# Kernel optimization log

Hardware: AMD Instinct MI355X
Metric: run time of the kernel (lower is better)

The kernel has to match this reference:

```python
import jax, jax.numpy as jnp
import numpy as np
from jax.scipy.special import gammaln

D = 512       # feature_dim
C = 64        # n classes (n-way)
SHOTS = 5     # matches hardcoded self.fix_Nj = 5
Q = 2048      # query samples
FIX_NJ = 5.0


def setup_inputs() -> dict:
    key = jax.random.key(0)
    k1, k2 = jax.random.split(key, 2)
    X_support = jax.random.normal(k1, (C * SHOTS, D), dtype=jnp.float32)
    # labels 0..C-1, SHOTS contiguous samples per class (required: code indexes mu[j] by label)
    y = (jnp.arange(C * SHOTS, dtype=jnp.int32) // SHOTS)
    X_query = jax.random.normal(k2, (Q, D), dtype=jnp.float32)
    # learned parameters, initialized exactly as in the torch module
    m = jnp.zeros((1, D), dtype=jnp.float32)
    kappa = jnp.float32(0.1)
    nu = jnp.float32(D)
    triu_S_diag = jnp.ones((D,), dtype=jnp.float32)
    triu_S_lower = jnp.eye(D, dtype=jnp.float32)
    return {"X_support": X_support, "y": y, "X_query": X_query,
            "m": m, "kappa": kappa, "nu": nu,
            "triu_S_diag": triu_S_diag, "triu_S_lower": triu_S_lower}


def reference(X_support, y, X_query, m, kappa, nu, triu_S_diag, triu_S_lower):
    # ---- compute_shared_part ----
    # triu(ones,1).t() == strictly-lower-triangular mask
    mask = jnp.tril(jnp.ones((D, D), dtype=X_support.dtype), -1)
    L = jnp.diag(jnp.abs(triu_S_diag)) + triu_S_lower * mask
    kappa_n = jnp.abs(kappa) + 1e-6 + FIX_NJ
    m_with_weight = jnp.abs(kappa + 1e-6) / kappa_n * m          # [1,D]
    xmean_weight = FIX_NJ / kappa_n
    scatter = L @ L.T                                            # self_outer(L), square case
    sp = jnp.clip(nu, D - 1 + 1e-6) + FIX_NJ - D + 2             # sharedpart (scalar)
    bias_shared = gammaln(0.5 * (sp + D)) - gammaln(0.5 * sp) - 0.5 * D * jnp.log(sp)

    # ---- fit_image_label, batched over classes ----
    # y is arange//SHOTS so grouping X[y==j] == contiguous reshape
    Xc = X_support.reshape(C, SHOTS, D)                          # [C,S,D]
    x_mean = Xc.mean(axis=1)                                     # [C,D]
    mean_outer = jnp.einsum('csd,cse->cde', Xc, Xc) / SHOTS      # X_j^T X_j / N_j
    mu = m_with_weight + x_mean * xmean_weight                   # [C,D]
    dm = x_mean - m                                              # [C,D]; self_outer of [1,D] row -> outer product
    sigma = scatter[None] + mean_outer \
        + jnp.einsum('cd,ce->cde', dm, dm) * ((jnp.abs(kappa) + 1e-6) / kappa_n)
    sigma = sigma / ((kappa_n + 1) / (kappa_n * sp))             # [C,D,D]
    sigma_inv = jnp.linalg.inv(sigma)                            # batched inverse
    _, logdet = jnp.linalg.slogdet(sigma)                        # sigma is PD -> logdet
    biases = bias_shared - 0.5 * logdet                          # [C]

    # ---- predict, batched over queries and classes ----
    diff = X_query[:, None, :] - mu[None, :, :]                  # [Q,C,D]
    tmp = jnp.einsum('qcd,cde->qce', diff, sigma_inv)
    dist = jnp.sum(tmp * diff, axis=-1)                          # Mahalanobis [Q,C]
    return biases[None, :] - 0.5 * (sp + D) * jnp.log(1.0 + dist / sp)
```

## Files before the change

kernel.cpp:

```cpp
#include <hip/hip_runtime.h>
#include <math.h>

#define D 512
#define NC 64
#define NQ 2048

typedef unsigned short u16;
typedef __attribute__((ext_vector_type(8))) short bf8;
typedef __attribute__((ext_vector_type(4))) float f4;

#define OFF_S    0
#define OFF_ABH  32
#define OFF_ABL  (OFF_ABH + 655360)
#define OFF_LH   (OFF_ABL + 655360)
#define OFF_LL   (OFF_LH + 131072)
#define OFF_WH   (OFF_LL + 131072)
#define OFF_WL   (OFF_WH + 131072)
#define OFF_YYH  (OFF_WL + 131072)
#define OFF_YYL  (OFF_YYH + 655360)
#define OFF_AQ   (OFF_YYL + 655360)
#define OFF_GRAM (OFF_AQ + NQ)

#define GIX(i, j) ((i) * 7 - (i) * ((i) + 1) / 2 + (j))

__device__ inline float wred(float v) {
#pragma unroll
  for (int off = 32; off; off >>= 1) v += __shfl_down(v, off);
  return v;
}

__device__ inline void split2(float v, u16& h, u16& l) {
  unsigned u = __float_as_uint(v);
  h = (u16)(u >> 16);
  float hf = __uint_as_float(u & 0xFFFF0000u);
  float r = v - hf;
  unsigned ru = __float_as_uint(r);
  l = (u16)((ru + 0x7FFFu + ((ru >> 16) & 1u)) >> 16);
}

__device__ inline void split4(float a0, float a1, float a2, float a3,
                              ushort4& h, ushort4& l) {
  u16 hh, ll;
  split2(a0, hh, ll); h.x = hh; l.x = ll;
  split2(a1, hh, ll); h.y = hh; l.y = ll;
  split2(a2, hh, ll); h.z = hh; l.z = ll;
  split2(a3, hh, ll); h.w = hh; l.w = ll;
}

#define MPAD 68
template <int N>
__device__ inline void lds_mm(float (*M)[MPAD], int ar, int ac, int br, int bc,
                              int cr, int cc, bool neg) {
  const int T = N / 16;
  int tx = (threadIdx.x & 15) * T, ty = (threadIdx.x >> 4) * T;
  float acc[T][T];
#pragma unroll
  for (int i = 0; i < T; ++i)
#pragma unroll
    for (int j = 0; j < T; ++j) acc[i][j] = 0.f;
#pragma unroll 8
  for (int k = 0; k < N; ++k) {
    float a[T], b[T];
#pragma unroll
    for (int i = 0; i < T; ++i) a[i] = M[ar + ty + i][ac + k];
#pragma unroll
    for (int j = 0; j < T; ++j) b[j] = M[br + k][bc + tx + j];
#pragma unroll
    for (int i = 0; i < T; ++i)
#pragma unroll
      for (int j = 0; j < T; ++j) acc[i][j] += a[i] * b[j];
  }
#pragma unroll
  for (int i = 0; i < T; ++i)
#pragma unroll
    for (int j = 0; j < T; ++j)
      M[cr + ty + i][cc + tx + j] = neg ? -acc[i][j] : acc[i][j];
}

__device__ inline void inv64(float (*M)[MPAD], int tid) {
  {
    float x[16];
    int q = tid >> 4, col = tid & 15;
    if (tid < 64) {
      int b = q << 4;
#pragma unroll
      for (int i = 0; i < 16; ++i) {
        float acc = 0.f;
#pragma unroll
        for (int k = 0; k < i; ++k) acc += M[b + i][b + k] * x[k];
        x[i] = (((i == col) ? 1.f : 0.f) - acc) / M[b + i][b + i];
      }
    }
    __syncthreads();
    if (tid < 64) {
      int b = q << 4;
#pragma unroll
      for (int i = 0; i < 16; ++i) M[b + i][b + col] = x[i];
    }
    __syncthreads();
  }
  for (int pp = 0; pp < 2; ++pp) {
    int r0 = 32 * pp;
    lds_mm<16>(M, r0 + 16, r0, r0, r0, r0, r0 + 16, false);
  }
  __syncthreads();
  for (int pp = 0; pp < 2; ++pp) {
    int r0 = 32 * pp;
    lds_mm<16>(M, r0 + 16, r0 + 16, r0, r0 + 16, r0 + 16, r0, true);
  }
  __syncthreads();
  for (int idx = tid; idx < 512; idx += 256) {
    int t2 = idx >> 8, r = (idx >> 4) & 15, c = idx & 15;
    M[32 * t2 + r][32 * t2 + 16 + c] = 0.f;
  }
  __syncthreads();
  lds_mm<32>(M, 32, 0, 0, 0, 0, 32, false);
  __syncthreads();
  lds_mm<32>(M, 32, 32, 0, 32, 32, 0, true);
  __syncthreads();
  for (int idx = tid; idx < 1024; idx += 256) {
    int r = idx >> 5, c = idx & 31;
    M[r][32 + c] = 0.f;
  }
  __syncthreads();
}

__global__ __launch_bounds__(256) void k_prep(const float* __restrict__ diag,
                                              const float* __restrict__ low,
                                              const float* __restrict__ Xs,
                                              const float* __restrict__ Xq,
                                              const float* __restrict__ m,
                                              const float* __restrict__ kp,
                                              const float* __restrict__ nup,
                                              u16* __restrict__ Lh, u16* __restrict__ Ll,
                                              u16* __restrict__ ABh, u16* __restrict__ ABl,
                                              u16* __restrict__ Wh, u16* __restrict__ Wl,
                                              float* __restrict__ S, float* __restrict__ aq,
                                              float* __restrict__ Gram) {
  __shared__ float M[64][MPAD];
  int bid = blockIdx.x, tid = threadIdx.x;
  if (bid < 8) {
    int p = bid * 64;
    for (int idx = tid; idx < 4096; idx += 256) {
      int r = idx >> 6, c = idx & 63;
      float v;
      if (r == c)      v = fabsf(diag[p + r]);
      else if (r > c)  v = low[(size_t)(p + r) * D + p + c];
      else             v = 0.f;
      M[r][c] = v;
    }
    __syncthreads();
    inv64(M, tid);
    for (int idx = tid; idx < 1024; idx += 256) {
      int r = idx >> 4, c4 = (idx & 15) << 2;
      ushort4 hh, ll;
      split4(M[r][c4 + 0], M[r][c4 + 1], M[r][c4 + 2], M[r][c4 + 3], hh, ll);
      size_t gi = (size_t)(p + r) * D + p + c4;
      *reinterpret_cast<ushort4*>(Wh + gi) = hh;
      *reinterpret_cast<ushort4*>(Wl + gi) = ll;
    }
  } else if (bid < 72) {
    int c = bid - 8;
    if (tid < 128) {
      float kappa = kp[0];
      float kn = fabsf(kappa) + 1e-6f + 5.0f;
      float xw = 5.0f / kn;
      float mw = fabsf(kappa + 1e-6f) / kn;
      float sw = sqrtf((fabsf(kappa) + 1e-6f) / kn);
      const float is5 = 0.44721359549995793f;
      int d4 = tid;
      float xs[5][4];
#pragma unroll
      for (int s = 0; s < 5; ++s) {
        float4 v = reinterpret_cast<const float4*>(Xs + (size_t)(c * 5 + s) * D)[d4];
        xs[s][0] = v.x; xs[s][1] = v.y; xs[s][2] = v.z; xs[s][3] = v.w;
      }
      float4 mvv = reinterpret_cast<const float4*>(m)[d4];
      float mv[4] = {mvv.x, mvv.y, mvv.z, mvv.w};
      float rows[8][4];
#pragma unroll
      for (int e = 0; e < 4; ++e) {
        float xm = (xs[0][e] + xs[1][e] + xs[2][e] + xs[3][e] + xs[4][e]) * 0.2f;
#pragma unroll
        for (int s = 0; s < 5; ++s) rows[s][e] = xs[s][e] * is5;
        rows[5][e] = sw * (xm - mv[e]);
        rows[6][e] = mw * mv[e] + xw * xm;
        rows[7][e] = 0.f;
      }
#pragma unroll
      for (int s = 0; s < 8; ++s) {
        ushort4 hh, ll;
        split4(rows[s][0], rows[s][1], rows[s][2], rows[s][3], hh, ll);
        size_t gi = (size_t)(c * 8 + s) * D + 4 * tid;
        *reinterpret_cast<ushort4*>(ABh + gi) = hh;
        *reinterpret_cast<ushort4*>(ABl + gi) = ll;
      }
    }
  } else if (bid == 72) {
    for (int i = tid; i < NQ; i += 256) aq[i] = 0.f;
    for (int i = tid; i < NC * 28; i += 256) Gram[i] = 0.f;
    if (tid >= 64) return;
    float part = 0.f;
    for (int i = tid; i < D; i += 64) part += logf(fabsf(diag[i]));
    part = wred(part);
    if (tid != 0) return;
    float lda = 2.f * part;
    float kappa = kp[0], nu = nup[0];
    float kn = fabsf(kappa) + 1e-6f + 5.0f;
    float sp = fmaxf(nu, (float)(D - 1) + 1e-6f) + 5.0f - (float)D + 2.0f;
    float bias_shared = lgammaf(0.5f * (sp + (float)D)) - lgammaf(0.5f * sp)
                      - 0.5f * (float)D * logf(sp);
    float scale = kn * sp / (kn + 1.0f);
    S[3] = bias_shared;
    S[8] = 1.f / scale;
    S[9] = (float)D * logf(scale) + lda;
    S[10] = 0.5f * (sp + (float)D);
    S[11] = 1.f / sp;
  } else if (bid < 329) {
    int t = (bid - 73) * 1024 + tid * 4;
    int i = t >> 9, j = t & 511;
    float4 lv = *reinterpret_cast<const float4*>(low + t);
    float a[4] = {lv.x, lv.y, lv.z, lv.w};
    float dv = diag[i];
    float o[4];
#pragma unroll
    for (int e = 0; e < 4; ++e) {
      int jj = j + e;
      o[e] = (i == jj) ? fabsf(dv) : (i > jj ? a[e] : 0.f);
    }
    ushort4 hh, ll;
    split4(o[0], o[1], o[2], o[3], hh, ll);
    *reinterpret_cast<ushort4*>(Lh + t) = hh;
    *reinterpret_cast<ushort4*>(Ll + t) = ll;
  } else {
    size_t base = (size_t)(bid - 329) * 8192;
#pragma unroll
    for (int it = 0; it < 8; ++it) {
      size_t idx = base + it * 1024 + tid * 4;
      float4 v = *reinterpret_cast<const float4*>(Xq + idx);
      ushort4 hh, ll;
      split4(v.x, v.y, v.z, v.w, hh, ll);
      *reinterpret_cast<ushort4*>(ABh + (size_t)512 * D + idx) = hh;
      *reinterpret_cast<ushort4*>(ABl + (size_t)512 * D + idx) = ll;
    }
  }
}

__global__ __launch_bounds__(256) void k_solve(const u16* __restrict__ Lh,
                                               const u16* __restrict__ Ll,
                                               u16* __restrict__ Wh,
                                               const u16* __restrict__ Wl) {
  __shared__ __align__(16) u16 XTh[32][520];
  __shared__ __align__(16) u16 XTl[32][520];
  __shared__ __align__(16) u16 STh[32][72];
  __shared__ __align__(16) u16 STl[32][72];
  int J = blockIdx.x;
  int i0 = J >> 1;
  int tid = threadIdx.x, w = tid >> 6, lane = tid & 63;
  int lr = lane & 15, kq = lane >> 4;
  for (int idx = tid; idx < 64 * 32; idx += 256) {
    int r = idx >> 5, c = idx & 31;
    size_t gi = (size_t)(64 * i0 + r) * D + 64 * i0 + (J & 1) * 32 + c;
    XTh[c][64 * i0 + r] = Wh[gi];
    XTl[c][64 * i0 + r] = Wl[gi];
  }
  __syncthreads();
  for (int i = i0 + 1; i < 8; ++i) {
    f4 acc[2];
    acc[0] = (f4){0.f, 0.f, 0.f, 0.f};
    acc[1] = (f4){0.f, 0.f, 0.f, 0.f};
    for (int k = i0; k < i; ++k) {
#pragma unroll
      for (int kk = 0; kk < 2; ++kk) {
        size_t ga = (size_t)(64 * i + w * 16 + lr) * D + 64 * k + kk * 32 + kq * 8;
        bf8 ah = *reinterpret_cast<const bf8*>(Lh + ga);
        bf8 al = *reinterpret_cast<const bf8*>(Ll + ga);
#pragma unroll
        for (int nf = 0; nf < 2; ++nf) {
          bf8 bh = *reinterpret_cast<const bf8*>(&XTh[nf * 16 + lr][64 * k + kk * 32 + kq * 8]);
          bf8 bl = *reinterpret_cast<const bf8*>(&XTl[nf * 16 + lr][64 * k + kk * 32 + kq * 8]);
          acc[nf] = __builtin_amdgcn_mfma_f32_16x16x32_bf16(ah, bh, acc[nf], 0, 0, 0);
          acc[nf] = __builtin_amdgcn_mfma_f32_16x16x32_bf16(ah, bl, acc[nf], 0, 0, 0);
          acc[nf] = __builtin_amdgcn_mfma_f32_16x16x32_bf16(al, bh, acc[nf], 0, 0, 0);
        }
      }
    }
#pragma unroll
    for (int nf = 0; nf < 2; ++nf)
#pragma unroll
      for (int reg = 0; reg < 4; ++reg) {
        float v = -acc[nf][reg];
        u16 hh, ll; split2(v, hh, ll);
        int c = nf * 16 + lr, r = w * 16 + kq * 4 + reg;
        STh[c][r] = hh; STl[c][r] = ll;
      }
    __syncthreads();
    f4 acc2[2];
    acc2[0] = (f4){0.f, 0.f, 0.f, 0.f};
    acc2[1] = (f4){0.f, 0.f, 0.f, 0.f};
#pragma unroll
    for (int kk = 0; kk < 2; ++kk) {
      size_t ga = (size_t)(64 * i + w * 16 + lr) * D + 64 * i + kk * 32 + kq * 8;
      bf8 ah = *reinterpret_cast<const bf8*>(Wh + ga);
      bf8 al = *reinterpret_cast<const bf8*>(Wl + ga);
#pragma unroll
      for (int nf = 0; nf < 2; ++nf) {
        bf8 bh = *reinterpret_cast<const bf8*>(&STh[nf * 16 + lr][kk * 32 + kq * 8]);
        bf8 bl = *reinterpret_cast<const bf8*>(&STl[nf * 16 + lr][kk * 32 + kq * 8]);
        acc2[nf] = __builtin_amdgcn_mfma_f32_16x16x32_bf16(ah, bh, acc2[nf], 0, 0, 0);
        acc2[nf] = __builtin_amdgcn_mfma_f32_16x16x32_bf16(ah, bl, acc2[nf], 0, 0, 0);
        acc2[nf] = __builtin_amdgcn_mfma_f32_16x16x32_bf16(al, bh, acc2[nf], 0, 0, 0);
      }
    }
#pragma unroll
    for (int nf = 0; nf < 2; ++nf)
#pragma unroll
      for (int reg = 0; reg < 4; ++reg) {
        float v = acc2[nf][reg];
        u16 hh, ll; split2(v, hh, ll);
        int r = w * 16 + kq * 4 + reg, c = nf * 16 + lr;
        Wh[(size_t)(64 * i + r) * D + 32 * J + c] = hh;
        XTh[c][64 * i + r] = hh; XTl[c][64 * i + r] = ll;
      }
    __syncthreads();
  }
}

__global__ __launch_bounds__(256) void k_mf1(const u16* __restrict__ ABh, const u16* __restrict__ ABl,
                                             const u16* __restrict__ Wh,
                                             u16* __restrict__ YYh, u16* __restrict__ YYl,
                                             float* __restrict__ Gram, float* __restrict__ aq) {
  __shared__ float Csh[64][68];
  int tid = threadIdx.x, w = tid >> 6, lane = tid & 63;
  int bn = (7 - (int)blockIdx.x) * 64;
  int m0 = blockIdx.y * 64 + w * 16;
  int lr = lane & 15, kof = (lane >> 4) * 8;
  const u16* ah_p = ABh + (size_t)(m0 + lr) * D + kof;
  const u16* al_p = ABl + (size_t)(m0 + lr) * D + kof;
  const u16* bh_p = Wh + (size_t)(bn + lr) * D + kof;
  f4 acc[4];
#pragma unroll
  for (int nf = 0; nf < 4; ++nf) acc[nf] = (f4){0.f, 0.f, 0.f, 0.f};
  int Klim = bn + 64;
#pragma unroll 2
  for (int k0 = 0; k0 < Klim; k0 += 32) {
    bf8 ah = *reinterpret_cast<const bf8*>(ah_p + k0);
    bf8 al = *reinterpret_cast<const bf8*>(al_p + k0);
    bf8 bh[4];
#pragma unroll
    for (int nf = 0; nf < 4; ++nf)
      bh[nf] = *reinterpret_cast<const bf8*>(bh_p + (size_t)nf * 16 * D + k0);
#pragma unroll
    for (int nf = 0; nf < 4; ++nf)
      acc[nf] = __builtin_amdgcn_mfma_f32_16x16x32_bf16(ah, bh[nf], acc[nf], 0, 0, 0);
#pragma unroll
    for (int nf = 0; nf < 4; ++nf)
      acc[nf] = __builtin_amdgcn_mfma_f32_16x16x32_bf16(al, bh[nf], acc[nf], 0, 0, 0);
  }
  int rbase = m0 + ((lane >> 4) << 2);
#pragma unroll
  for (int reg = 0; reg < 4; ++reg) {
    int row = rbase + reg;
    float sq = 0.f;
#pragma unroll
    for (int nf = 0; nf < 4; ++nf) {
      float v = acc[nf][reg];
      size_t gi = (size_t)row * D + bn + nf * 16 + lr;
      u16 hh, ll; split2(v, hh, ll);
      YYh[gi] = hh;
      if (row >= 512) YYl[gi] = ll;
      sq += v * v;
    }
    if (row >= 512) {
#pragma unroll
      for (int mk = 1; mk < 16; mk <<= 1) sq += __shfl_xor(sq, mk);
      if (lr == 0) atomicAdd(&aq[row - 512], sq);
    }
  }
  if (blockIdx.y < 8) {
#pragma unroll
    for (int reg = 0; reg < 4; ++reg)
#pragma unroll
      for (int nf = 0; nf < 4; ++nf)
        Csh[w * 16 + ((lane >> 4) << 2) + reg][nf * 16 + lr] = acc[nf][reg];
    __syncthreads();
    if (tid < 224) {
      const int PI[28] = {0,0,0,0,0,0,0, 1,1,1,1,1,1, 2,2,2,2,2, 3,3,3,3, 4,4,4, 5,5, 6};
      const int PJ[28] = {0,1,2,3,4,5,6, 1,2,3,4,5,6, 2,3,4,5,6, 3,4,5,6, 4,5,6, 5,6, 6};
      int cl = tid / 28, p = tid % 28;
      const float* ri = Csh[cl * 8 + PI[p]];
      const float* rj = Csh[cl * 8 + PJ[p]];
      float s = 0.f;
#pragma unroll
      for (int c4 = 0; c4 < 64; c4 += 4) {
        float4 a = *reinterpret_cast<const float4*>(&ri[c4]);
        float4 b = *reinterpret_cast<const float4*>(&rj[c4]);
        s += a.x * b.x + a.y * b.y + a.z * b.z + a.w * b.w;
      }
      atomicAdd(&Gram[(blockIdx.y * 8 + cl) * 28 + p], s);
    }
  }
}

__global__ __launch_bounds__(256) void k_mf2(const u16* __restrict__ Yh, const u16* __restrict__ Yl,
                                             const u16* __restrict__ Bh,
                                             const float* __restrict__ aq,
                                             const float* __restrict__ Gram,
                                             const float* __restrict__ S,
                                             float* __restrict__ out) {
  __shared__ float Csh[4][16][68];
  __shared__ float PRo[8][15], PRd[8][6], Psv[8][6], Pb[8], Ph[8];
  int tid = threadIdx.x, w = tid >> 6, lane = tid & 63;
  int m0 = blockIdx.x * 64 + w * 16;
  int bn = blockIdx.y * 64;
  int lr = lane & 15, kof = (lane >> 4) * 8;
  const u16* ah_p = Yh + (size_t)(m0 + lr) * D + kof;
  const u16* al_p = Yl + (size_t)(m0 + lr) * D + kof;
  const u16* bh_p = Bh + (size_t)(bn + lr) * D + kof;
  f4 acc[4];
#pragma unroll
  for (int nf = 0; nf < 4; ++nf) acc[nf] = (f4){0.f, 0.f, 0.f, 0.f};
#pragma unroll 2
  for (int k0 = 0; k0 < D; k0 += 32) {
    bf8 ah = *reinterpret_cast<const bf8*>(ah_p + k0);
    bf8 al = *reinterpret_cast<const bf8*>(al_p + k0);
    bf8 bh[4];
#pragma unroll
    for (int nf = 0; nf < 4; ++nf)
      bh[nf] = *reinterpret_cast<const bf8*>(bh_p + (size_t)nf * 16 * D + k0);
#pragma unroll
    for (int nf = 0; nf < 4; ++nf)
      acc[nf] = __builtin_amdgcn_mfma_f32_16x16x32_bf16(ah, bh[nf], acc[nf], 0, 0, 0);
#pragma unroll
    for (int nf = 0; nf < 4; ++nf)
      acc[nf] = __builtin_amdgcn_mfma_f32_16x16x32_bf16(al, bh[nf], acc[nf], 0, 0, 0);
  }
#pragma unroll
  for (int reg = 0; reg < 4; ++reg)
#pragma unroll
    for (int nf = 0; nf < 4; ++nf)
      Csh[w][((lane >> 4) << 2) + reg][nf * 16 + lr] = acc[nf][reg];
  if (tid < 8) {
    int c = blockIdx.y * 8 + tid;
    float Gv[28];
#pragma unroll
    for (int p = 0; p < 28; ++p) Gv[p] = Gram[c * 28 + p];
    float R[6][6];
    float logdetM = 0.f;
#pragma unroll
    for (int i = 0; i < 6; ++i) {
      float s = Gv[GIX(i, i)] + 1.f;
#pragma unroll
      for (int k = 0; k < i; ++k) s -= R[i][k] * R[i][k];
      float rii = sqrtf(s);
      R[i][i] = rii;
      logdetM += logf(rii);
      float inv = 1.f / rii;
      PRd[tid][i] = inv;
#pragma unroll
      for (int r = i + 1; r < 6; ++r) {
        float s2 = Gv[GIX(i, r)];
#pragma unroll
        for (int k = 0; k < i; ++k) s2 -= R[r][k] * R[i][k];
        R[r][i] = s2 * inv;
      }
    }
#pragma unroll
    for (int i = 1; i < 6; ++i)
#pragma unroll
      for (int k = 0; k < i; ++k)
        PRo[tid][i * (i - 1) / 2 + k] = R[i][k];
#pragma unroll
    for (int j = 0; j < 6; ++j) Psv[tid][j] = Gv[GIX(j, 6)];
    Ph[tid] = Gv[27];
    Pb[tid] = S[3] - 0.5f * (S[9] + 2.f * logdetM);
  }
  __syncthreads();
  float s8 = S[8], s10 = S[10], s11 = S[11];
  int r = lr;
  int q = m0 + r;
  float aqv = aq[q];
#pragma unroll
  for (int cc = 0; cc < 2; ++cc) {
    int cl = ((lane >> 4) << 1) + cc;
    const float* t = &Csh[w][r][cl * 8];
    float e[6];
#pragma unroll
    for (int j = 0; j < 6; ++j) e[j] = t[j] - Psv[cl][j];
    const float* o = PRo[cl];
    const float* dg = PRd[cl];
    float z0 = e[0] * dg[0];
    float z1 = (e[1] - o[0] * z0) * dg[1];
    float z2 = (e[2] - o[1] * z0 - o[2] * z1) * dg[2];
    float z3 = (e[3] - o[3] * z0 - o[4] * z1 - o[5] * z2) * dg[3];
    float z4 = (e[4] - o[6] * z0 - o[7] * z1 - o[8] * z2 - o[9] * z3) * dg[4];
    float z5 = (e[5] - o[10] * z0 - o[11] * z1 - o[12] * z2 - o[13] * z3 - o[14] * z4) * dg[5];
    float quad = z0 * z0 + z1 * z1 + z2 * z2 + z3 * z3 + z4 * z4 + z5 * z5;
    float dist = (aqv - 2.f * t[6] + Ph[cl] - quad) * s8;
    out[(size_t)q * NC + blockIdx.y * 8 + cl] = Pb[cl] - s10 * log1pf(dist * s11);
  }
}

extern "C" void kernel_launch(void* const* d_in, const int* in_sizes, int n_in,
                              void* d_out, int out_size, void* d_ws, size_t ws_size,
                              hipStream_t stream) {
  const float* Xs   = (const float*)d_in[0];
  const float* Xq   = (const float*)d_in[2];
  const float* m    = (const float*)d_in[3];
  const float* kap  = (const float*)d_in[4];
  const float* nu   = (const float*)d_in[5];
  const float* diag = (const float*)d_in[6];
  const float* low  = (const float*)d_in[7];
  float* ws = (float*)d_ws;

  float* S    = ws + OFF_S;
  u16*   ABh  = (u16*)(ws + OFF_ABH);
  u16*   ABl  = (u16*)(ws + OFF_ABL);
  u16*   Lh   = (u16*)(ws + OFF_LH);
  u16*   Ll   = (u16*)(ws + OFF_LL);
  u16*   Wh   = (u16*)(ws + OFF_WH);
  u16*   Wl   = (u16*)(ws + OFF_WL);
  u16*   YYh  = (u16*)(ws + OFF_YYH);
  u16*   YYl  = (u16*)(ws + OFF_YYL);
  float* aq   = ws + OFF_AQ;
  float* Gram = ws + OFF_GRAM;

  hipLaunchKernelGGL(k_prep, dim3(457), dim3(256), 0, stream,
                     diag, low, Xs, Xq, m, kap, nu, Lh, Ll, ABh, ABl, Wh, Wl, S, aq, Gram);
  hipLaunchKernelGGL(k_solve, dim3(16), dim3(256), 0, stream, Lh, Ll, Wh, Wl);
  hipLaunchKernelGGL(k_mf1, dim3(8, 40), dim3(256), 0, stream,
                     ABh, ABl, Wh, YYh, YYl, Gram, aq);
  hipLaunchKernelGGL(k_mf2, dim3(32, 8), dim3(256), 0, stream,
                     YYh + (size_t)512 * D, YYl + (size_t)512 * D, YYh,
                     aq, Gram, S, (float*)d_out);
}
```

Before: 88.79 us.

## Replace explicit L inverse and GEMM with fused blockwise triangular solve

Instead of forming the full inverse of L (k_solve) and then multiplying the support and query rows by it (k_mf1), each block now loads 32 rows into LDS and does a blocked forward substitution using L and the inverted 64x64 diagonal blocks. The Gram partial sums and query squared norms are computed in the same kernel, and the prep kernel no longer writes the bf16 split copies of the inputs. This drops one launch and several global round trips. In exchange only 80 blocks run a serial 8-step dependency chain with many barriers, so the GPU may be underfilled.

```diff
diff --git a/kernel.cpp b/kernel.cpp
--- a/kernel.cpp
+++ b/kernel.cpp
@@ -10,13 +10,11 @@
 typedef __attribute__((ext_vector_type(4))) float f4;
 
 #define OFF_S    0
-#define OFF_ABH  32
-#define OFF_ABL  (OFF_ABH + 655360)
-#define OFF_LH   (OFF_ABL + 655360)
+#define OFF_LH   32
 #define OFF_LL   (OFF_LH + 131072)
-#define OFF_WH   (OFF_LL + 131072)
-#define OFF_WL   (OFF_WH + 131072)
-#define OFF_YYH  (OFF_WL + 131072)
+#define OFF_DIH  (OFF_LL + 131072)
+#define OFF_DIL  (OFF_DIH + 16384)
+#define OFF_YYH  (OFF_DIL + 16384)
 #define OFF_YYL  (OFF_YYH + 655360)
 #define OFF_AQ   (OFF_YYL + 655360)
 #define OFF_GRAM (OFF_AQ + NQ)
@@ -47,6 +45,10 @@
   split2(a3, hh, ll); h.w = hh; l.w = ll;
 }
 
+__device__ inline float recon(u16 h, u16 l) {
+  return __uint_as_float((unsigned)h << 16) + __uint_as_float((unsigned)l << 16);
+}
+
 #define MPAD 68
 template <int N>
 __device__ inline void lds_mm(float (*M)[MPAD], int ar, int ac, int br, int bc,
@@ -127,16 +129,11 @@
 
 __global__ __launch_bounds__(256) void k_prep(const float* __restrict__ diag,
                                               const float* __restrict__ low,
-                                              const float* __restrict__ Xs,
-                                              const float* __restrict__ Xq,
-                                              const float* __restrict__ m,
                                               const float* __restrict__ kp,
                                               const float* __restrict__ nup,
                                               u16* __restrict__ Lh, u16* __restrict__ Ll,
-                                              u16* __restrict__ ABh, u16* __restrict__ ABl,
-                                              u16* __restrict__ Wh, u16* __restrict__ Wl,
-                                              float* __restrict__ S, float* __restrict__ aq,
-                                              float* __restrict__ Gram) {
+                                              u16* __restrict__ DIh, u16* __restrict__ DIl,
+                                              float* __restrict__ S) {
   __shared__ float M[64][MPAD];
   int bid = blockIdx.x, tid = threadIdx.x;
   if (bid < 8) {
@@ -155,50 +152,27 @@
       int r = idx >> 4, c4 = (idx & 15) << 2;
       ushort4 hh, ll;
       split4(M[r][c4 + 0], M[r][c4 + 1], M[r][c4 + 2], M[r][c4 + 3], hh, ll);
-      size_t gi = (size_t)(p + r) * D + p + c4;
-      *reinterpret_cast<ushort4*>(Wh + gi) = hh;
-      *reinterpret_cast<ushort4*>(Wl + gi) = ll;
-    }
-  } else if (bid < 72) {
-    int c = bid - 8;
-    if (tid < 128) {
-      float kappa = kp[0];
-      float kn = fabsf(kappa) + 1e-6f + 5.0f;
-      float xw = 5.0f / kn;
-      float mw = fabsf(kappa + 1e-6f) / kn;
-      float sw = sqrtf((fabsf(kappa) + 1e-6f) / kn);
-      const float is5 = 0.44721359549995793f;
-      int d4 = tid;
-      float xs[5][4];
-#pragma unroll
-      for (int s = 0; s < 5; ++s) {
-        float4 v = reinterpret_cast<const float4*>(Xs + (size_t)(c * 5 + s) * D)[d4];
-        xs[s][0] = v.x; xs[s][1] = v.y; xs[s][2] = v.z; xs[s][3] = v.w;
-      }
-      float4 mvv = reinterpret_cast<const float4*>(m)[d4];
-      float mv[4] = {mvv.x, mvv.y, mvv.z, mvv.w};
-      float rows[8][4];
-#pragma unroll
-      for (int e = 0; e < 4; ++e) {
-        float xm = (xs[0][e] + xs[1][e] + xs[2][e] + xs[3][e] + xs[4][e]) * 0.2f;
-#pragma unroll
-        for (int s = 0; s < 5; ++s) rows[s][e] = xs[s][e] * is5;
-        rows[5][e] = sw * (xm - mv[e]);
-        rows[6][e] = mw * mv[e] + xw * xm;
-        rows[7][e] = 0.f;
-      }
-#pragma unroll
-      for (int s = 0; s < 8; ++s) {
-        ushort4 hh, ll;
-        split4(rows[s][0], rows[s][1], rows[s][2], rows[s][3], hh, ll);
-        size_t gi = (size_t)(c * 8 + s) * D + 4 * tid;
-        *reinterpret_cast<ushort4*>(ABh + gi) = hh;
-        *reinterpret_cast<ushort4*>(ABl + gi) = ll;
-      }
-    }
-  } else if (bid == 72) {
-    for (int i = tid; i < NQ; i += 256) aq[i] = 0.f;
-    for (int i = tid; i < NC * 28; i += 256) Gram[i] = 0.f;
+      size_t gi = (size_t)bid * 4096 + r * 64 + c4;
+      *reinterpret_cast<ushort4*>(DIh + gi) = hh;
+      *reinterpret_cast<ushort4*>(DIl + gi) = ll;
+    }
+  } else if (bid < 264) {
+    int t = (bid - 8) * 1024 + tid * 4;
+    int i = t >> 9, j = t & 511;
+    float4 lv = *reinterpret_cast<const float4*>(low + t);
+    float a[4] = {lv.x, lv.y, lv.z, lv.w};
+    float dv = diag[i];
+    float o[4];
+#pragma unroll
+    for (int e = 0; e < 4; ++e) {
+      int jj = j + e;
+      o[e] = (i == jj) ? fabsf(dv) : (i > jj ? a[e] : 0.f);
+    }
+    ushort4 hh, ll;
+    split4(o[0], o[1], o[2], o[3], hh, ll);
+    *reinterpret_cast<ushort4*>(Lh + t) = hh;
+    *reinterpret_cast<ushort4*>(Ll + t) = ll;
+  } else {
     if (tid >= 64) return;
     float part = 0.f;
     for (int i = tid; i < D; i += 64) part += logf(fabsf(diag[i]));
@@ -216,72 +190,98 @@
     S[9] = (float)D * logf(scale) + lda;
     S[10] = 0.5f * (sp + (float)D);
     S[11] = 1.f / sp;
-  } else if (bid < 329) {
-    int t = (bid - 73) * 1024 + tid * 4;
-    int i = t >> 9, j = t & 511;
-    float4 lv = *reinterpret_cast<const float4*>(low + t);
-    float a[4] = {lv.x, lv.y, lv.z, lv.w};
-    float dv = diag[i];
-    float o[4];
-#pragma unroll
-    for (int e = 0; e < 4; ++e) {
-      int jj = j + e;
-      o[e] = (i == jj) ? fabsf(dv) : (i > jj ? a[e] : 0.f);
-    }
-    ushort4 hh, ll;
-    split4(o[0], o[1], o[2], o[3], hh, ll);
-    *reinterpret_cast<ushort4*>(Lh + t) = hh;
-    *reinterpret_cast<ushort4*>(Ll + t) = ll;
+  }
+}
+
+__global__ __launch_bounds__(256) void k_fsolve(const u16* __restrict__ Lh,
+                                                const u16* __restrict__ Ll,
+                                                const u16* __restrict__ DIh,
+                                                const u16* __restrict__ DIl,
+                                                const float* __restrict__ Xs,
+                                                const float* __restrict__ Xq,
+                                                const float* __restrict__ m,
+                                                const float* __restrict__ kp,
+                                                u16* __restrict__ YYh, u16* __restrict__ YYl,
+                                                float* __restrict__ Gram,
+                                                float* __restrict__ aq) {
+  __shared__ __align__(16) u16 Yhs[32][536];
+  __shared__ __align__(16) u16 Yls[32][536];
+  __shared__ __align__(16) float Ts[32][68];
+  __shared__ float asq[32];
+  int bid = blockIdx.x, tid = threadIdx.x;
+  int w = tid >> 6, lane = tid & 63;
+  int lr = lane & 15, kq = lane >> 4;
+  int mi = w >> 1, nb0 = (w & 1) * 2;
+  bool isU = bid < 16;
+  int row0 = bid * 32;
+  if (isU) {
+    float kappa = kp[0];
+    float kn = fabsf(kappa) + 1e-6f + 5.0f;
+    float xw = 5.0f / kn;
+    float mw = fabsf(kappa + 1e-6f) / kn;
+    float sw = sqrtf((fabsf(kappa) + 1e-6f) / kn);
+    const float is5 = 0.44721359549995793f;
+    for (int d = tid; d < D; d += 256) {
+      float mv = m[d];
+#pragma unroll
+      for (int cl = 0; cl < 4; ++cl) {
+        int c = bid * 4 + cl;
+        float x0 = Xs[(size_t)(c * 5 + 0) * D + d];
+        float x1 = Xs[(size_t)(c * 5 + 1) * D + d];
+        float x2 = Xs[(size_t)(c * 5 + 2) * D + d];
+        float x3 = Xs[(size_t)(c * 5 + 3) * D + d];
+        float x4 = Xs[(size_t)(c * 5 + 4) * D + d];
+        float xm = (x0 + x1 + x2 + x3 + x4) * 0.2f;
+        float rows[8];
+        rows[0] = x0 * is5; rows[1] = x1 * is5; rows[2] = x2 * is5;
+        rows[3] = x3 * is5; rows[4] = x4 * is5;
+        rows[5] = sw * (xm - mv);
+        rows[6] = mw * mv + xw * xm;
+        rows[7] = 0.f;
+#pragma unroll
+        for (int s = 0; s < 8; ++s) {
+          u16 hh, ll; split2(rows[s], hh, ll);
+          Yhs[cl * 8 + s][d] = hh; Yls[cl * 8 + s][d] = ll;
+        }
+      }
+    }
   } else {
-    size_t base = (size_t)(bid - 329) * 8192;
-#pragma unroll
-    for (int it = 0; it < 8; ++it) {
-      size_t idx = base + it * 1024 + tid * 4;
-      float4 v = *reinterpret_cast<const float4*>(Xq + idx);
-      ushort4 hh, ll;
-      split4(v.x, v.y, v.z, v.w, hh, ll);
-      *reinterpret_cast<ushort4*>(ABh + (size_t)512 * D + idx) = hh;
-      *reinterpret_cast<ushort4*>(ABl + (size_t)512 * D + idx) = ll;
-    }
-  }
-}
-
-__global__ __launch_bounds__(256) void k_solve(const u16* __restrict__ Lh,
-                                               const u16* __restrict__ Ll,
-                                               u16* __restrict__ Wh,
-                                               const u16* __restrict__ Wl) {
-  __shared__ __align__(16) u16 XTh[32][520];
-  __shared__ __align__(16) u16 XTl[32][520];
-  __shared__ __align__(16) u16 STh[32][72];
-  __shared__ __align__(16) u16 STl[32][72];
-  int J = blockIdx.x;
-  int i0 = J >> 1;
-  int tid = threadIdx.x, w = tid >> 6, lane = tid & 63;
-  int lr = lane & 15, kq = lane >> 4;
-  for (int idx = tid; idx < 64 * 32; idx += 256) {
-    int r = idx >> 5, c = idx & 31;
-    size_t gi = (size_t)(64 * i0 + r) * D + 64 * i0 + (J & 1) * 32 + c;
-    XTh[c][64 * i0 + r] = Wh[gi];
-    XTl[c][64 * i0 + r] = Wl[gi];
-  }
-  __syncthreads();
-  for (int i = i0 + 1; i < 8; ++i) {
+    int q0 = row0 - 512;
+    for (int idx = tid; idx < 32 * 128; idx += 256) {
+      int r = idx >> 7, c4 = (idx & 127) << 2;
+      float4 v = *reinterpret_cast<const float4*>(&Xq[(size_t)(q0 + r) * D + c4]);
+      u16 hh, ll;
+      split2(v.x, hh, ll); Yhs[r][c4 + 0] = hh; Yls[r][c4 + 0] = ll;
+      split2(v.y, hh, ll); Yhs[r][c4 + 1] = hh; Yls[r][c4 + 1] = ll;
+      split2(v.z, hh, ll); Yhs[r][c4 + 2] = hh; Yls[r][c4 + 2] = ll;
+      split2(v.w, hh, ll); Yhs[r][c4 + 3] = hh; Yls[r][c4 + 3] = ll;
+    }
+    if (tid < 32) asq[tid] = 0.f;
+  }
+  __syncthreads();
+  const int PI[28] = {0,0,0,0,0,0,0, 1,1,1,1,1,1, 2,2,2,2,2, 3,3,3,3, 4,4,4, 5,5, 6};
+  const int PJ[28] = {0,1,2,3,4,5,6, 1,2,3,4,5,6, 2,3,4,5,6, 3,4,5,6, 4,5,6, 5,6, 6};
+  int gcl = tid / 28, gp = tid % 28;
+  float gacc = 0.f;
+  float sqs[4] = {0.f, 0.f, 0.f, 0.f};
+  for (int i = 0; i < 8; ++i) {
     f4 acc[2];
     acc[0] = (f4){0.f, 0.f, 0.f, 0.f};
     acc[1] = (f4){0.f, 0.f, 0.f, 0.f};
-    for (int k = i0; k < i; ++k) {
+    for (int k = 0; k < i; ++k) {
 #pragma unroll
       for (int kk = 0; kk < 2; ++kk) {
-        size_t ga = (size_t)(64 * i + w * 16 + lr) * D + 64 * k + kk * 32 + kq * 8;
-        bf8 ah = *reinterpret_cast<const bf8*>(Lh + ga);
-        bf8 al = *reinterpret_cast<const bf8*>(Ll + ga);
+        int co = 64 * k + kk * 32 + kq * 8;
+        bf8 ah = *reinterpret_cast<const bf8*>(&Yhs[16 * mi + lr][co]);
+        bf8 al = *reinterpret_cast<const bf8*>(&Yls[16 * mi + lr][co]);
 #pragma unroll
         for (int nf = 0; nf < 2; ++nf) {
-          bf8 bh = *reinterpret_cast<const bf8*>(&XTh[nf * 16 + lr][64 * k + kk * 32 + kq * 8]);
-          bf8 bl = *reinterpret_cast<const bf8*>(&XTl[nf * 16 + lr][64 * k + kk * 32 + kq * 8]);
+          size_t gb = (size_t)(64 * i + (nb0 + nf) * 16 + lr) * D + co;
+          bf8 bh = *reinterpret_cast<const bf8*>(Lh + gb);
+          bf8 bl = *reinterpret_cast<const bf8*>(Ll + gb);
           acc[nf] = __builtin_amdgcn_mfma_f32_16x16x32_bf16(ah, bh, acc[nf], 0, 0, 0);
+          acc[nf] = __builtin_amdgcn_mfma_f32_16x16x32_bf16(al, bh, acc[nf], 0, 0, 0);
           acc[nf] = __builtin_amdgcn_mfma_f32_16x16x32_bf16(ah, bl, acc[nf], 0, 0, 0);
-          acc[nf] = __builtin_amdgcn_mfma_f32_16x16x32_bf16(al, bh, acc[nf], 0, 0, 0);
         }
       }
     }
@@ -289,10 +289,9 @@
     for (int nf = 0; nf < 2; ++nf)
 #pragma unroll
       for (int reg = 0; reg < 4; ++reg) {
-        float v = -acc[nf][reg];
-        u16 hh, ll; split2(v, hh, ll);
-        int c = nf * 16 + lr, r = w * 16 + kq * 4 + reg;
-        STh[c][r] = hh; STl[c][r] = ll;
+        int rl = 16 * mi + kq * 4 + reg, cl_ = (nb0 + nf) * 16 + lr;
+        float ab = recon(Yhs[rl][64 * i + cl_], Yls[rl][64 * i + cl_]);
+        Ts[rl][cl_] = ab - acc[nf][reg];
       }
     __syncthreads();
     f4 acc2[2];
@@ -300,105 +299,67 @@
     acc2[1] = (f4){0.f, 0.f, 0.f, 0.f};
 #pragma unroll
     for (int kk = 0; kk < 2; ++kk) {
-      size_t ga = (size_t)(64 * i + w * 16 + lr) * D + 64 * i + kk * 32 + kq * 8;
-      bf8 ah = *reinterpret_cast<const bf8*>(Wh + ga);
-      bf8 al = *reinterpret_cast<const bf8*>(Wl + ga);
+      int co = kk * 32 + kq * 8;
+      float4 t0 = *reinterpret_cast<const float4*>(&Ts[16 * mi + lr][co]);
+      float4 t1 = *reinterpret_cast<const float4*>(&Ts[16 * mi + lr][co + 4]);
+      float tv[8] = {t0.x, t0.y, t0.z, t0.w, t1.x, t1.y, t1.z, t1.w};
+      bf8 ah2, al2;
+#pragma unroll
+      for (int e = 0; e < 8; ++e) {
+        u16 hh, ll; split2(tv[e], hh, ll);
+        ah2[e] = (short)hh; al2[e] = (short)ll;
+      }
 #pragma unroll
       for (int nf = 0; nf < 2; ++nf) {
-        bf8 bh = *reinterpret_cast<const bf8*>(&STh[nf * 16 + lr][kk * 32 + kq * 8]);
-        bf8 bl = *reinterpret_cast<const bf8*>(&STl[nf * 16 + lr][kk * 32 + kq * 8]);
-        acc2[nf] = __builtin_amdgcn_mfma_f32_16x16x32_bf16(ah, bh, acc2[nf], 0, 0, 0);
-        acc2[nf] = __builtin_amdgcn_mfma_f32_16x16x32_bf16(ah, bl, acc2[nf], 0, 0, 0);
-        acc2[nf] = __builtin_amdgcn_mfma_f32_16x16x32_bf16(al, bh, acc2[nf], 0, 0, 0);
-      }
-    }
+        size_t db = (size_t)i * 4096 + ((nb0 + nf) * 16 + lr) * 64 + co;
+        bf8 bh = *reinterpret_cast<const bf8*>(DIh + db);
+        bf8 bl = *reinterpret_cast<const bf8*>(DIl + db);
+        acc2[nf] = __builtin_amdgcn_mfma_f32_16x16x32_bf16(ah2, bh, acc2[nf], 0, 0, 0);
+        acc2[nf] = __builtin_amdgcn_mfma_f32_16x16x32_bf16(al2, bh, acc2[nf], 0, 0, 0);
+        acc2[nf] = __builtin_amdgcn_mfma_f32_16x16x32_bf16(ah2, bl, acc2[nf], 0, 0, 0);
+      }
+    }
+    __syncthreads();
 #pragma unroll
     for (int nf = 0; nf < 2; ++nf)
 #pragma unroll
       for (int reg = 0; reg < 4; ++reg) {
+        int rl = 16 * mi + kq * 4 + reg, cl_ = (nb0 + nf) * 16 + lr;
         float v = acc2[nf][reg];
         u16 hh, ll; split2(v, hh, ll);
-        int r = w * 16 + kq * 4 + reg, c = nf * 16 + lr;
-        Wh[(size_t)(64 * i + r) * D + 32 * J + c] = hh;
-        XTh[c][64 * i + r] = hh; XTl[c][64 * i + r] = ll;
-      }
-    __syncthreads();
-  }
-}
-
-__global__ __launch_bounds__(256) void k_mf1(const u16* __restrict__ ABh, const u16* __restrict__ ABl,
-                                             const u16* __restrict__ Wh,
-                                             u16* __restrict__ YYh, u16* __restrict__ YYl,
-                                             float* __restrict__ Gram, float* __restrict__ aq) {
-  __shared__ float Csh[64][68];
-  int tid = threadIdx.x, w = tid >> 6, lane = tid & 63;
-  int bn = (7 - (int)blockIdx.x) * 64;
-  int m0 = blockIdx.y * 64 + w * 16;
-  int lr = lane & 15, kof = (lane >> 4) * 8;
-  const u16* ah_p = ABh + (size_t)(m0 + lr) * D + kof;
-  const u16* al_p = ABl + (size_t)(m0 + lr) * D + kof;
-  const u16* bh_p = Wh + (size_t)(bn + lr) * D + kof;
-  f4 acc[4];
-#pragma unroll
-  for (int nf = 0; nf < 4; ++nf) acc[nf] = (f4){0.f, 0.f, 0.f, 0.f};
-  int Klim = bn + 64;
-#pragma unroll 2
-  for (int k0 = 0; k0 < Klim; k0 += 32) {
-    bf8 ah = *reinterpret_cast<const bf8*>(ah_p + k0);
-    bf8 al = *reinterpret_cast<const bf8*>(al_p + k0);
-    bf8 bh[4];
-#pragma unroll
-    for (int nf = 0; nf < 4; ++nf)
-      bh[nf] = *reinterpret_cast<const bf8*>(bh_p + (size_t)nf * 16 * D + k0);
-#pragma unroll
-    for (int nf = 0; nf < 4; ++nf)
-      acc[nf] = __builtin_amdgcn_mfma_f32_16x16x32_bf16(ah, bh[nf], acc[nf], 0, 0, 0);
-#pragma unroll
-    for (int nf = 0; nf < 4; ++nf)
-      acc[nf] = __builtin_amdgcn_mfma_f32_16x16x32_bf16(al, bh[nf], acc[nf], 0, 0, 0);
-  }
-  int rbase = m0 + ((lane >> 4) << 2);
-#pragma unroll
-  for (int reg = 0; reg < 4; ++reg) {
-    int row = rbase + reg;
-    float sq = 0.f;
-#pragma unroll
-    for (int nf = 0; nf < 4; ++nf) {
-      float v = acc[nf][reg];
-      size_t gi = (size_t)row * D + bn + nf * 16 + lr;
-      u16 hh, ll; split2(v, hh, ll);
-      YYh[gi] = hh;
-      if (row >= 512) YYl[gi] = ll;
-      sq += v * v;
-    }
-    if (row >= 512) {
-#pragma unroll
-      for (int mk = 1; mk < 16; mk <<= 1) sq += __shfl_xor(sq, mk);
-      if (lr == 0) atomicAdd(&aq[row - 512], sq);
-    }
-  }
-  if (blockIdx.y < 8) {
-#pragma unroll
-    for (int reg = 0; reg < 4; ++reg)
-#pragma unroll
-      for (int nf = 0; nf < 4; ++nf)
-        Csh[w * 16 + ((lane >> 4) << 2) + reg][nf * 16 + lr] = acc[nf][reg];
-    __syncthreads();
-    if (tid < 224) {
-      const int PI[28] = {0,0,0,0,0,0,0, 1,1,1,1,1,1, 2,2,2,2,2, 3,3,3,3, 4,4,4, 5,5, 6};
-      const int PJ[28] = {0,1,2,3,4,5,6, 1,2,3,4,5,6, 2,3,4,5,6, 3,4,5,6, 4,5,6, 5,6, 6};
-      int cl = tid / 28, p = tid % 28;
-      const float* ri = Csh[cl * 8 + PI[p]];
-      const float* rj = Csh[cl * 8 + PJ[p]];
-      float s = 0.f;
-#pragma unroll
-      for (int c4 = 0; c4 < 64; c4 += 4) {
-        float4 a = *reinterpret_cast<const float4*>(&ri[c4]);
-        float4 b = *reinterpret_cast<const float4*>(&rj[c4]);
-        s += a.x * b.x + a.y * b.y + a.z * b.z + a.w * b.w;
-      }
-      atomicAdd(&Gram[(blockIdx.y * 8 + cl) * 28 + p], s);
-    }
+        Yhs[rl][64 * i + cl_] = hh; Yls[rl][64 * i + cl_] = ll;
+        size_t gi = (size_t)(row0 + rl) * D + 64 * i + cl_;
+        YYh[gi] = hh;
+        if (!isU) { YYl[gi] = ll; sqs[reg] += v * v; }
+        else Ts[rl][cl_] = v;
+      }
+    if (isU) {
+      __syncthreads();
+      if (tid < 112) {
+        const float* ri = Ts[gcl * 8 + PI[gp]];
+        const float* rj = Ts[gcl * 8 + PJ[gp]];
+        float s = 0.f;
+#pragma unroll
+        for (int c4 = 0; c4 < 64; c4 += 4) {
+          float4 a = *reinterpret_cast<const float4*>(&ri[c4]);
+          float4 b = *reinterpret_cast<const float4*>(&rj[c4]);
+          s += a.x * b.x + a.y * b.y + a.z * b.z + a.w * b.w;
+        }
+        gacc += s;
+      }
+    }
+    __syncthreads();
+  }
+  if (isU) {
+    if (tid < 112) Gram[((size_t)bid * 4 + gcl) * 28 + gp] = gacc;
+  } else {
+#pragma unroll
+    for (int reg = 0; reg < 4; ++reg) {
+      int rl = 16 * mi + kq * 4 + reg;
+      atomicAdd(&asq[rl], sqs[reg]);
+    }
+    __syncthreads();
+    if (tid < 32) aq[row0 - 512 + tid] = asq[tid];
   }
 }
 
@@ -514,22 +475,19 @@
   float* ws = (float*)d_ws;
 
   float* S    = ws + OFF_S;
-  u16*   ABh  = (u16*)(ws + OFF_ABH);
-  u16*   ABl  = (u16*)(ws + OFF_ABL);
   u16*   Lh   = (u16*)(ws + OFF_LH);
   u16*   Ll   = (u16*)(ws + OFF_LL);
-  u16*   Wh   = (u16*)(ws + OFF_WH);
-  u16*   Wl   = (u16*)(ws + OFF_WL);
+  u16*   DIh  = (u16*)(ws + OFF_DIH);
+  u16*   DIl  = (u16*)(ws + OFF_DIL);
   u16*   YYh  = (u16*)(ws + OFF_YYH);
   u16*   YYl  = (u16*)(ws + OFF_YYL);
   float* aq   = ws + OFF_AQ;
   float* Gram = ws + OFF_GRAM;
 
-  hipLaunchKernelGGL(k_prep, dim3(457), dim3(256), 0, stream,
-                     diag, low, Xs, Xq, m, kap, nu, Lh, Ll, ABh, ABl, Wh, Wl, S, aq, Gram);
-  hipLaunchKernelGGL(k_solve, dim3(16), dim3(256), 0, stream, Lh, Ll, Wh, Wl);
-  hipLaunchKernelGGL(k_mf1, dim3(8, 40), dim3(256), 0, stream,
-                     ABh, ABl, Wh, YYh, YYl, Gram, aq);
+  hipLaunchKernelGGL(k_prep, dim3(265), dim3(256), 0, stream,
+                     diag, low, kap, nu, Lh, Ll, DIh, DIl, S);
+  hipLaunchKernelGGL(k_fsolve, dim3(80), dim3(256), 0, stream,
+                     Lh, Ll, DIh, DIl, Xs, Xq, m, kap, YYh, YYl, Gram, aq);
   hipLaunchKernelGGL(k_mf2, dim3(32, 8), dim3(256), 0, stream,
                      YYh + (size_t)512 * D, YYl + (size_t)512 * D, YYh,
                      aq, Gram, S, (float*)d_out);
```

Result: no change. 90.15 us (+1.5%).
